# Optimization experiments

Measured on AMD Instinct MI355X. Metric: run time of the kernel, lower is better.

The kernel has to match this reference:

```python
import jax, jax.numpy as jnp
import numpy as np

NUM_NODES = 100000
EMBED_DIM = 64
NUM_LAYERS = 3
NUM_EDGES = 1250000
NUM_LABEL = 1000000


def setup_inputs() -> dict:
    key = jax.random.key(0)
    k1, k2, k3 = jax.random.split(key, 3)
    edge_index = jax.random.randint(k1, (2, NUM_EDGES), 0, NUM_NODES, dtype=jnp.int64)
    edge_label_index = jax.random.randint(k2, (2, NUM_LABEL), 0, NUM_NODES, dtype=jnp.int64)
    emb = jax.random.normal(k3, (NUM_NODES, EMBED_DIM), dtype=jnp.float32)
    # LightGCN default: uniform alpha = 1/(num_layers+1)
    alpha = jnp.full((NUM_LAYERS + 1,), 1.0 / (NUM_LAYERS + 1), dtype=jnp.float32)
    return {"edge_index": edge_index, "edge_label_index": edge_label_index,
            "emb": emb, "alpha": alpha}


def reference(edge_index, edge_label_index, emb, alpha):
    row, col = edge_index[0], edge_index[1]  # src -> dst
    # symmetric GCN normalization without self-loops (LGConv default)
    ones = jnp.ones(row.shape, dtype=emb.dtype)
    deg = jax.ops.segment_sum(ones, col, num_segments=NUM_NODES)  # [N]
    dinv = jnp.where(deg > 0, jax.lax.rsqrt(deg), jnp.zeros_like(deg))
    norm = dinv[row] * dinv[col]  # [E]

    # layer-wise linear propagation + alpha-weighted sum
    x = emb
    out = alpha[0] * x
    for l in range(NUM_LAYERS):
        msg = x[row] * norm[:, None]                     # gather + scale [E, d]
        x = jax.ops.segment_sum(msg, col, num_segments=NUM_NODES)  # scatter-add [N, d]
        out = out + alpha[l + 1] * x

    # dot-product ranking on label edges
    src = out[edge_label_index[0]]  # [E_label, d]
    dst = out[edge_label_index[1]]
    return jnp.sum(src * dst, axis=-1)  # [E_label]
```

## Files before the change

kernel.cpp:

```cpp
#include <hip/hip_runtime.h>

#define NN 100000
#define DIM 64
#define NE 1250000
#define NL 1000000
#define CAP 64

#define NBKT 196
#define CAPB 8192
#define A_EPT 16
#define A_EPB (256 * A_EPT)

typedef unsigned int   u32;
typedef unsigned short u16;

__device__ inline u32 pack2bf(float lo, float hi) {
    u32 a = __float_as_uint(lo); a = (a + 0x7FFFu + ((a >> 16) & 1u)) >> 16;
    u32 b = __float_as_uint(hi); b = (b + 0x7FFFu + ((b >> 16) & 1u)) & 0xFFFF0000u;
    return a | b;
}
__device__ inline float blo(u32 w) { return __uint_as_float(w << 16); }
__device__ inline float bhi(u32 w) { return __uint_as_float(w & 0xFFFF0000u); }

__global__ void k_part(const int* __restrict__ row, const int* __restrict__ col,
                       int* __restrict__ bcnt, u32* __restrict__ bedges) {
    __shared__ int hist[256];
    __shared__ int sbase[257];
    __shared__ int cur[256];
    __shared__ int gbase[256];
    __shared__ u32 stag[A_EPB];
    int t = threadIdx.x;
    hist[t] = 0; cur[t] = 0;
    __syncthreads();

    int base = blockIdx.x * A_EPB;
    int myc[A_EPT], myr[A_EPT];
    #pragma unroll
    for (int j = 0; j < A_EPT; ++j) {
        int e = base + j * 256 + t;
        if (e < NE) {
            myc[j] = col[e]; myr[j] = row[e];
            atomicAdd(&hist[myc[j] >> 9], 1);
        } else myc[j] = -1;
    }
    __syncthreads();

    int v = hist[t];
    sbase[t] = v;
    __syncthreads();
    for (int s = 1; s < 256; s <<= 1) {
        int add = (t >= s) ? sbase[t - s] : 0;
        __syncthreads();
        sbase[t] += add;
        __syncthreads();
    }
    int incl = sbase[t];
    __syncthreads();
    sbase[t] = incl - v;
    if (t == 255) sbase[256] = incl;
    if (t < NBKT && v > 0) gbase[t] = atomicAdd(&bcnt[t], v);
    __syncthreads();

    #pragma unroll
    for (int j = 0; j < A_EPT; ++j) {
        if (myc[j] >= 0) {
            int b = myc[j] >> 9;
            int r = atomicAdd(&cur[b], 1);
            stag[sbase[b] + r] = ((u32)myr[j] << 9) | (u32)(myc[j] & 511);
        }
    }
    __syncthreads();

    int total = sbase[256];
    for (int p = t; p < total; p += 256) {
        int lo = 0, hi = 255;
        while (lo < hi) {
            int mid = (lo + hi + 1) >> 1;
            if (sbase[mid] <= p) lo = mid; else hi = mid - 1;
        }
        int gi = gbase[lo] + (p - sbase[lo]);
        if (gi < CAPB) bedges[(size_t)lo * CAPB + gi] = stag[p];
    }
}

__global__ void k_bucket(const int* __restrict__ bcnt, const u32* __restrict__ bedges,
                         int* __restrict__ deg, int* __restrict__ csr) {
    __shared__ int hist[512];
    __shared__ int curb[512];
    int b = blockIdx.x, t = threadIdx.x;
    int cnt = bcnt[b]; if (cnt > CAPB) cnt = CAPB;
    int node0 = b << 9;
    for (int i = t; i < 512; i += 256) { hist[i] = 0; curb[i] = 0; }
    __syncthreads();

    u32 my[CAPB / 256];
    #pragma unroll
    for (int j = 0; j < CAPB / 256; ++j) {
        int idx = j * 256 + t;
        if (idx < cnt) {
            my[j] = bedges[(size_t)b * CAPB + idx];
            atomicAdd(&hist[my[j] & 511], 1);
        }
    }
    __syncthreads();

    for (int i = t; i < 512; i += 256) {
        int n = node0 + i;
        if (n < NN) deg[n] = hist[i] < CAP ? hist[i] : CAP;
    }

    #pragma unroll
    for (int j = 0; j < CAPB / 256; ++j) {
        int idx = j * 256 + t;
        if (idx < cnt) {
            int lc = my[j] & 511;
            int r = atomicAdd(&curb[lc], 1);
            if (r < CAP) csr[((size_t)(node0 + lc) << 6) + r] = (int)(my[j] >> 9);
        }
    }
}

__global__ void k_init(const float* __restrict__ emb, const int* __restrict__ deg,
                       u16* __restrict__ y0) {
    int i = blockIdx.x * blockDim.x + threadIdx.x;
    if (i < NN * DIM / 4) {
        int n = i >> 4;
        float d = (float)deg[n];
        float di = d > 0.f ? rsqrtf(d) : 0.f;
        float4 v = ((const float4*)emb)[i];
        uint2 p;
        p.x = pack2bf(di * v.x, di * v.y);
        p.y = pack2bf(di * v.z, di * v.w);
        ((uint2*)y0)[i] = p;
    }
}

__global__ void k_g(const int* __restrict__ deg, const int* __restrict__ csr,
                    const u16* __restrict__ yin, u16* __restrict__ yout) {
    int t = blockIdx.x * blockDim.x + threadIdx.x;
    int node = t >> 3;
    if (node >= NN) return;
    int k = t & 7;
    int d = deg[node];
    int cnt = d < CAP ? d : CAP;
    const int* base = csr + ((size_t)node << 6);

    float s[8];
    #pragma unroll
    for (int j = 0; j < 8; ++j) s[j] = 0.f;

    for (int b = 0; b < cnt; b += 8) {
        int nb = cnt - b; if (nb > 8) nb = 8;
        int my = (b + k < cnt) ? base[b + k] : 0;
        uint4 v[8];
        #pragma unroll
        for (int j = 0; j < 8; ++j) {
            int src = __shfl(my, j, 8);
            if (j < nb) v[j] = ((const uint4*)(yin + (size_t)src * DIM))[k];
            else { v[j].x = 0u; v[j].y = 0u; v[j].z = 0u; v[j].w = 0u; }
        }
        #pragma unroll
        for (int j = 0; j < 8; ++j) {
            s[0] += blo(v[j].x); s[1] += bhi(v[j].x);
            s[2] += blo(v[j].y); s[3] += bhi(v[j].y);
            s[4] += blo(v[j].z); s[5] += bhi(v[j].z);
            s[6] += blo(v[j].w); s[7] += bhi(v[j].w);
        }
    }
    float df = (float)d;
    float di = d > 0 ? rsqrtf(df) : 0.f;
    float di2 = di * di;
    uint4 yn;
    yn.x = pack2bf(di2 * s[0], di2 * s[1]);
    yn.y = pack2bf(di2 * s[2], di2 * s[3]);
    yn.z = pack2bf(di2 * s[4], di2 * s[5]);
    yn.w = pack2bf(di2 * s[6], di2 * s[7]);
    ((uint4*)(yout + (size_t)node * DIM))[k] = yn;
}

__global__ void k_g3(const int* __restrict__ deg, const int* __restrict__ csr,
                     const u16* __restrict__ yin,
                     const u16* __restrict__ y1, const u16* __restrict__ y2,
                     const float* __restrict__ emb, const float* __restrict__ alpha,
                     u16* __restrict__ accB) {
    int t = blockIdx.x * blockDim.x + threadIdx.x;
    int node = t >> 3;
    if (node >= NN) return;
    int k = t & 7;
    int d = deg[node];
    int cnt = d < CAP ? d : CAP;
    const int* base = csr + ((size_t)node << 6);

    float s[8];
    #pragma unroll
    for (int j = 0; j < 8; ++j) s[j] = 0.f;

    for (int b = 0; b < cnt; b += 8) {
        int nb = cnt - b; if (nb > 8) nb = 8;
        int my = (b + k < cnt) ? base[b + k] : 0;
        uint4 v[8];
        #pragma unroll
        for (int j = 0; j < 8; ++j) {
            int src = __shfl(my, j, 8);
            if (j < nb) v[j] = ((const uint4*)(yin + (size_t)src * DIM))[k];
            else { v[j].x = 0u; v[j].y = 0u; v[j].z = 0u; v[j].w = 0u; }
        }
        #pragma unroll
        for (int j = 0; j < 8; ++j) {
            s[0] += blo(v[j].x); s[1] += bhi(v[j].x);
            s[2] += blo(v[j].y); s[3] += bhi(v[j].y);
            s[4] += blo(v[j].z); s[5] += bhi(v[j].z);
            s[6] += blo(v[j].w); s[7] += bhi(v[j].w);
        }
    }
    float df = (float)d;
    float di  = d > 0 ? rsqrtf(df) : 0.f;
    float rdi = sqrtf(df);
    float a0 = alpha[0], a1 = alpha[1], a2 = alpha[2], a3 = alpha[3];

    size_t rowOff = (size_t)node * DIM;
    const float4* pe = (const float4*)(emb + rowOff);
    float4 e0 = pe[2 * k], e1 = pe[2 * k + 1];
    uint4 w1 = ((const uint4*)(y1 + rowOff))[k];
    uint4 w2 = ((const uint4*)(y2 + rowOff))[k];

    float o[8];
    o[0] = a0 * e0.x + a1 * rdi * blo(w1.x) + a2 * rdi * blo(w2.x) + a3 * di * s[0];
    o[1] = a0 * e0.y + a1 * rdi * bhi(w1.x) + a2 * rdi * bhi(w2.x) + a3 * di * s[1];
    o[2] = a0 * e0.z + a1 * rdi * blo(w1.y) + a2 * rdi * blo(w2.y) + a3 * di * s[2];
    o[3] = a0 * e0.w + a1 * rdi * bhi(w1.y) + a2 * rdi * bhi(w2.y) + a3 * di * s[3];
    o[4] = a0 * e1.x + a1 * rdi * blo(w1.z) + a2 * rdi * blo(w2.z) + a3 * di * s[4];
    o[5] = a0 * e1.y + a1 * rdi * bhi(w1.z) + a2 * rdi * bhi(w2.z) + a3 * di * s[5];
    o[6] = a0 * e1.z + a1 * rdi * blo(w1.w) + a2 * rdi * blo(w2.w) + a3 * di * s[6];
    o[7] = a0 * e1.w + a1 * rdi * bhi(w1.w) + a2 * rdi * bhi(w2.w) + a3 * di * s[7];

    uint4 fn;
    fn.x = pack2bf(o[0], o[1]);
    fn.y = pack2bf(o[2], o[3]);
    fn.z = pack2bf(o[4], o[5]);
    fn.w = pack2bf(o[6], o[7]);
    ((uint4*)(accB + rowOff))[k] = fn;
}

__global__ void k_dot(const int* __restrict__ s, const int* __restrict__ d,
                      const u16* __restrict__ emb, float* __restrict__ res) {
    int t = blockIdx.x * blockDim.x + threadIdx.x;
    int e = t >> 2;
    if (e >= NL) return;
    int k = t & 3;
    const uint4* pa = (const uint4*)(emb + (size_t)s[e] * DIM);
    const uint4* pb = (const uint4*)(emb + (size_t)d[e] * DIM);
    uint4 a0 = pa[k];
    uint4 a1 = pa[k + 4];
    uint4 b0 = pb[k];
    uint4 b1 = pb[k + 4];
    float p = blo(a0.x) * blo(b0.x) + bhi(a0.x) * bhi(b0.x)
            + blo(a0.y) * blo(b0.y) + bhi(a0.y) * bhi(b0.y)
            + blo(a0.z) * blo(b0.z) + bhi(a0.z) * bhi(b0.z)
            + blo(a0.w) * blo(b0.w) + bhi(a0.w) * bhi(b0.w)
            + blo(a1.x) * blo(b1.x) + bhi(a1.x) * bhi(b1.x)
            + blo(a1.y) * blo(b1.y) + bhi(a1.y) * bhi(b1.y)
            + blo(a1.z) * blo(b1.z) + bhi(a1.z) * bhi(b1.z)
            + blo(a1.w) * blo(b1.w) + bhi(a1.w) * bhi(b1.w);
    p += __shfl_down(p, 2, 4);
    p += __shfl_down(p, 1, 4);
    if (k == 0) res[e] = p;
}

extern "C" void kernel_launch(void* const* d_in, const int* in_sizes, int n_in,
                              void* d_out, int out_size, void* d_ws, size_t ws_size,
                              hipStream_t stream) {
    const int*   ei    = (const int*)d_in[0];
    const int*   eli   = (const int*)d_in[1];
    const float* emb   = (const float*)d_in[2];
    const float* alpha = (const float*)d_in[3];
    float* out = (float*)d_out;

    const int* row = ei;
    const int* col = ei + NE;
    const int* ls  = eli;
    const int* ld  = eli + NL;

    char* ws = (char*)d_ws;
    size_t o = 0;
    const size_t FEATB = (size_t)NN * DIM * sizeof(u16);
    int* deg    = (int*)(ws + o); o += 512 * 1024;
    int* bcnt   = (int*)(ws + o); o += 4 * 1024;
    u32* bedges = (u32*)(ws + o); o += (size_t)NBKT * CAPB * 4;
    int* csr    = (int*)(ws + o); o += (size_t)NN * CAP * 4;
    u16* y0     = (u16*)(ws + o); o += FEATB;
    u16* y1     = (u16*)(ws + o); o += FEATB;
    u16* y2     = (u16*)(ws + o); o += FEATB;
    u16* accB   = (u16*)(ws + o); o += FEATB;

    const int B = 256;
    const int gA   = (NE + A_EPB - 1) / A_EPB;
    const int gVec = (NN * DIM / 4 + B - 1) / B;
    const int gGat = ((NN * 8) + B - 1) / B;
    const int gDot = ((NL * 4) + B - 1) / B;

    hipMemsetAsync(bcnt, 0, NBKT * sizeof(int), stream);
    k_part<<<gA, B, 0, stream>>>(row, col, bcnt, bedges);
    k_bucket<<<NBKT, B, 0, stream>>>(bcnt, bedges, deg, csr);
    k_init<<<gVec, B, 0, stream>>>(emb, deg, y0);
    k_g<<<gGat, B, 0, stream>>>(deg, csr, y0, y1);
    k_g<<<gGat, B, 0, stream>>>(deg, csr, y1, y2);
    k_g3<<<gGat, B, 0, stream>>>(deg, csr, y2, y1, y2, emb, alpha, accB);
    k_dot<<<gDot, B, 0, stream>>>(ls, ld, accB, out);
}
```

Measured before the change: 164.4 us.

## Fuse y0 init into bucket kernel, replace binary search with LUT, reuse y0 in final layer

The partition kernel now records each staged edge's bucket id in a shared byte array, replacing the per-element binary search over bucket offsets. The bucket kernel now runs with 512 threads, one per node in its bucket. It also computes the scaled bf16 y0 directly from its shared histogram, so the separate init kernel launch and its degree reload go away. The final layer reconstructs the alpha0 term from bf16 y0 times sqrt(deg) instead of reading fp32 emb for nodes with degree, which halves that read but adds bf16 rounding error. Degree is no longer clamped to CAP when written, which changes normalization for nodes with more than 64 in-edges.

```diff
diff --git a/kernel.cpp b/kernel.cpp
--- a/kernel.cpp
+++ b/kernel.cpp
@@ -10,9 +10,11 @@
 #define CAPB 8192
 #define A_EPT 16
 #define A_EPB (256 * A_EPT)
+#define BKT_T 512
 
 typedef unsigned int   u32;
 typedef unsigned short u16;
+typedef unsigned char  u8;
 
 __device__ inline u32 pack2bf(float lo, float hi) {
     u32 a = __float_as_uint(lo); a = (a + 0x7FFFu + ((a >> 16) & 1u)) >> 16;
@@ -29,6 +31,7 @@
     __shared__ int cur[256];
     __shared__ int gbase[256];
     __shared__ u32 stag[A_EPB];
+    __shared__ u8  lutb[A_EPB];
     int t = threadIdx.x;
     hist[t] = 0; cur[t] = 0;
     __syncthreads();
@@ -66,72 +69,67 @@
         if (myc[j] >= 0) {
             int b = myc[j] >> 9;
             int r = atomicAdd(&cur[b], 1);
-            stag[sbase[b] + r] = ((u32)myr[j] << 9) | (u32)(myc[j] & 511);
+            int slot = sbase[b] + r;
+            stag[slot] = ((u32)myr[j] << 9) | (u32)(myc[j] & 511);
+            lutb[slot] = (u8)b;
         }
     }
     __syncthreads();
 
     int total = sbase[256];
     for (int p = t; p < total; p += 256) {
-        int lo = 0, hi = 255;
-        while (lo < hi) {
-            int mid = (lo + hi + 1) >> 1;
-            if (sbase[mid] <= p) lo = mid; else hi = mid - 1;
-        }
-        int gi = gbase[lo] + (p - sbase[lo]);
-        if (gi < CAPB) bedges[(size_t)lo * CAPB + gi] = stag[p];
+        int b = lutb[p];
+        int gi = gbase[b] + (p - sbase[b]);
+        if (gi < CAPB) bedges[(size_t)b * CAPB + gi] = stag[p];
     }
 }
 
 __global__ void k_bucket(const int* __restrict__ bcnt, const u32* __restrict__ bedges,
-                         int* __restrict__ deg, int* __restrict__ csr) {
+                         const float* __restrict__ emb,
+                         int* __restrict__ deg, int* __restrict__ csr,
+                         u16* __restrict__ y0) {
     __shared__ int hist[512];
     __shared__ int curb[512];
     int b = blockIdx.x, t = threadIdx.x;
     int cnt = bcnt[b]; if (cnt > CAPB) cnt = CAPB;
     int node0 = b << 9;
-    for (int i = t; i < 512; i += 256) { hist[i] = 0; curb[i] = 0; }
-    __syncthreads();
-
-    u32 my[CAPB / 256];
-    #pragma unroll
-    for (int j = 0; j < CAPB / 256; ++j) {
-        int idx = j * 256 + t;
+    hist[t] = 0; curb[t] = 0;
+    __syncthreads();
+
+    u32 my[CAPB / BKT_T];
+    #pragma unroll
+    for (int j = 0; j < CAPB / BKT_T; ++j) {
+        int idx = j * BKT_T + t;
         if (idx < cnt) {
             my[j] = bedges[(size_t)b * CAPB + idx];
             atomicAdd(&hist[my[j] & 511], 1);
-        }
-    }
-    __syncthreads();
-
-    for (int i = t; i < 512; i += 256) {
-        int n = node0 + i;
-        if (n < NN) deg[n] = hist[i] < CAP ? hist[i] : CAP;
-    }
-
-    #pragma unroll
-    for (int j = 0; j < CAPB / 256; ++j) {
-        int idx = j * 256 + t;
-        if (idx < cnt) {
+        } else my[j] = 0xFFFFFFFFu;
+    }
+    __syncthreads();
+
+    int n = node0 + t;
+    if (n < NN) deg[n] = hist[t];
+
+    for (int i = t; i < 512 * (DIM / 4); i += BKT_T) {
+        int ln = i >> 4;
+        int n2 = node0 + ln;
+        if (n2 >= NN) break;
+        float d = (float)hist[ln];
+        float di = d > 0.f ? rsqrtf(d) : 0.f;
+        float4 v = ((const float4*)emb)[(size_t)n2 * (DIM / 4) + (i & 15)];
+        uint2 p;
+        p.x = pack2bf(di * v.x, di * v.y);
+        p.y = pack2bf(di * v.z, di * v.w);
+        ((uint2*)y0)[(size_t)n2 * (DIM / 4) + (i & 15)] = p;
+    }
+
+    #pragma unroll
+    for (int j = 0; j < CAPB / BKT_T; ++j) {
+        if (my[j] != 0xFFFFFFFFu) {
             int lc = my[j] & 511;
             int r = atomicAdd(&curb[lc], 1);
             if (r < CAP) csr[((size_t)(node0 + lc) << 6) + r] = (int)(my[j] >> 9);
         }
-    }
-}
-
-__global__ void k_init(const float* __restrict__ emb, const int* __restrict__ deg,
-                       u16* __restrict__ y0) {
-    int i = blockIdx.x * blockDim.x + threadIdx.x;
-    if (i < NN * DIM / 4) {
-        int n = i >> 4;
-        float d = (float)deg[n];
-        float di = d > 0.f ? rsqrtf(d) : 0.f;
-        float4 v = ((const float4*)emb)[i];
-        uint2 p;
-        p.x = pack2bf(di * v.x, di * v.y);
-        p.y = pack2bf(di * v.z, di * v.w);
-        ((uint2*)y0)[i] = p;
     }
 }
 
@@ -179,7 +177,7 @@
 }
 
 __global__ void k_g3(const int* __restrict__ deg, const int* __restrict__ csr,
-                     const u16* __restrict__ yin,
+                     const u16* __restrict__ y0,
                      const u16* __restrict__ y1, const u16* __restrict__ y2,
                      const float* __restrict__ emb, const float* __restrict__ alpha,
                      u16* __restrict__ accB) {
@@ -202,7 +200,7 @@
         #pragma unroll
         for (int j = 0; j < 8; ++j) {
             int src = __shfl(my, j, 8);
-            if (j < nb) v[j] = ((const uint4*)(yin + (size_t)src * DIM))[k];
+            if (j < nb) v[j] = ((const uint4*)(y2 + (size_t)src * DIM))[k];
             else { v[j].x = 0u; v[j].y = 0u; v[j].z = 0u; v[j].w = 0u; }
         }
         #pragma unroll
@@ -219,20 +217,31 @@
     float a0 = alpha[0], a1 = alpha[1], a2 = alpha[2], a3 = alpha[3];
 
     size_t rowOff = (size_t)node * DIM;
-    const float4* pe = (const float4*)(emb + rowOff);
-    float4 e0 = pe[2 * k], e1 = pe[2 * k + 1];
+    float e[8];
+    if (d > 0) {
+        uint4 w0 = ((const uint4*)(y0 + rowOff))[k];
+        e[0] = rdi * blo(w0.x); e[1] = rdi * bhi(w0.x);
+        e[2] = rdi * blo(w0.y); e[3] = rdi * bhi(w0.y);
+        e[4] = rdi * blo(w0.z); e[5] = rdi * bhi(w0.z);
+        e[6] = rdi * blo(w0.w); e[7] = rdi * bhi(w0.w);
+    } else {
+        const float4* pe = (const float4*)(emb + rowOff);
+        float4 e0 = pe[2 * k], e1 = pe[2 * k + 1];
+        e[0] = e0.x; e[1] = e0.y; e[2] = e0.z; e[3] = e0.w;
+        e[4] = e1.x; e[5] = e1.y; e[6] = e1.z; e[7] = e1.w;
+    }
     uint4 w1 = ((const uint4*)(y1 + rowOff))[k];
     uint4 w2 = ((const uint4*)(y2 + rowOff))[k];
 
     float o[8];
-    o[0] = a0 * e0.x + a1 * rdi * blo(w1.x) + a2 * rdi * blo(w2.x) + a3 * di * s[0];
-    o[1] = a0 * e0.y + a1 * rdi * bhi(w1.x) + a2 * rdi * bhi(w2.x) + a3 * di * s[1];
-    o[2] = a0 * e0.z + a1 * rdi * blo(w1.y) + a2 * rdi * blo(w2.y) + a3 * di * s[2];
-    o[3] = a0 * e0.w + a1 * rdi * bhi(w1.y) + a2 * rdi * bhi(w2.y) + a3 * di * s[3];
-    o[4] = a0 * e1.x + a1 * rdi * blo(w1.z) + a2 * rdi * blo(w2.z) + a3 * di * s[4];
-    o[5] = a0 * e1.y + a1 * rdi * bhi(w1.z) + a2 * rdi * bhi(w2.z) + a3 * di * s[5];
-    o[6] = a0 * e1.z + a1 * rdi * blo(w1.w) + a2 * rdi * blo(w2.w) + a3 * di * s[6];
-    o[7] = a0 * e1.w + a1 * rdi * bhi(w1.w) + a2 * rdi * bhi(w2.w) + a3 * di * s[7];
+    o[0] = a0 * e[0] + a1 * rdi * blo(w1.x) + a2 * rdi * blo(w2.x) + a3 * di * s[0];
+    o[1] = a0 * e[1] + a1 * rdi * bhi(w1.x) + a2 * rdi * bhi(w2.x) + a3 * di * s[1];
+    o[2] = a0 * e[2] + a1 * rdi * blo(w1.y) + a2 * rdi * blo(w2.y) + a3 * di * s[2];
+    o[3] = a0 * e[3] + a1 * rdi * bhi(w1.y) + a2 * rdi * bhi(w2.y) + a3 * di * s[3];
+    o[4] = a0 * e[4] + a1 * rdi * blo(w1.z) + a2 * rdi * blo(w2.z) + a3 * di * s[4];
+    o[5] = a0 * e[5] + a1 * rdi * bhi(w1.z) + a2 * rdi * bhi(w2.z) + a3 * di * s[5];
+    o[6] = a0 * e[6] + a1 * rdi * blo(w1.w) + a2 * rdi * blo(w2.w) + a3 * di * s[6];
+    o[7] = a0 * e[7] + a1 * rdi * bhi(w1.w) + a2 * rdi * bhi(w2.w) + a3 * di * s[7];
 
     uint4 fn;
     fn.x = pack2bf(o[0], o[1]);
@@ -295,16 +304,14 @@
 
     const int B = 256;
     const int gA   = (NE + A_EPB - 1) / A_EPB;
-    const int gVec = (NN * DIM / 4 + B - 1) / B;
     const int gGat = ((NN * 8) + B - 1) / B;
     const int gDot = ((NL * 4) + B - 1) / B;
 
     hipMemsetAsync(bcnt, 0, NBKT * sizeof(int), stream);
     k_part<<<gA, B, 0, stream>>>(row, col, bcnt, bedges);
-    k_bucket<<<NBKT, B, 0, stream>>>(bcnt, bedges, deg, csr);
-    k_init<<<gVec, B, 0, stream>>>(emb, deg, y0);
+    k_bucket<<<NBKT, BKT_T, 0, stream>>>(bcnt, bedges, emb, deg, csr, y0);
     k_g<<<gGat, B, 0, stream>>>(deg, csr, y0, y1);
     k_g<<<gGat, B, 0, stream>>>(deg, csr, y1, y2);
-    k_g3<<<gGat, B, 0, stream>>>(deg, csr, y2, y1, y2, emb, alpha, accB);
+    k_g3<<<gGat, B, 0, stream>>>(deg, csr, y0, y1, y2, emb, alpha, accB);
     k_dot<<<gDot, B, 0, stream>>>(ls, ld, accB, out);
 }
```

New measurement: 150.8 us. 8.3% less time.
